# Optimization experiments

Hardware: AMD Instinct MI355X
Metric: run time of the kernel (lower is better)

## Reference

```python
import jax, jax.numpy as jnp
import numpy as np

EPS = 1e-6
H = 16  # num_heads

def _ln(x):
    mu = jnp.mean(x, axis=-1, keepdims=True)
    var = jnp.mean(jnp.square(x - mu), axis=-1, keepdims=True)
    return (x - mu) / jnp.sqrt(var + EPS)

def _mod(x, shift, scale):  # shift/scale: [B,D]
    return x * (1.0 + scale[:, None, :]) + shift[:, None, :]

def _heads(x, qkv_w, qkv_b):
    B, N, C = x.shape
    hd = C // H
    qkv = (x @ qkv_w + qkv_b).reshape(B, N, 3, H, hd).transpose(2, 0, 3, 1, 4)
    return qkv[0], qkv[1], qkv[2]  # each [B,H,N,hd]

def _attend(q, k, v):
    sc = (q.shape[-1]) ** -0.5
    a = jax.nn.softmax(jnp.einsum('bhnd,bhmd->bhnm', q, k) * sc, axis=-1)
    o = jnp.einsum('bhnm,bhmd->bhnd', a, v)
    B, h, N, hd = o.shape
    return o.transpose(0, 2, 1, 3).reshape(B, N, h * hd)

def _mha(x, qkv_w, qkv_b, proj_w, proj_b):
    q, k, v = _heads(x, qkv_w, qkv_b)
    return _attend(q, k, v) @ proj_w + proj_b

def setup_inputs() -> dict:
    key = jax.random.key(0)
    ks = jax.random.split(key, 16)
    B, T, D = 2, 2048, 1024
    Dh = 4 * D
    s = 0.02
    return {
        'x': jax.random.normal(ks[0], (B, T, D), jnp.float32),
        'c': jax.random.normal(ks[1], (B, 2, D), jnp.float32),
        'attn_qkv_w': jax.random.normal(ks[2], (D, 3 * D), jnp.float32) * s,
        'attn_qkv_b': jnp.zeros((3 * D,), jnp.float32),
        'attn_proj_w': jax.random.normal(ks[3], (D, D), jnp.float32) * s,
        'attn_proj_b': jnp.zeros((D,), jnp.float32),
        'crs_qkv_w': jax.random.normal(ks[4], (D, 3 * D), jnp.float32) * s,
        'crs_qkv_b': jnp.zeros((3 * D,), jnp.float32),
        'crs_proj_w': jax.random.normal(ks[5], (D, D), jnp.float32) * s,
        'crs_proj_b': jnp.zeros((D,), jnp.float32),
        'mlp_fc1_w': jax.random.normal(ks[6], (D, Dh), jnp.float32) * s,
        'mlp_fc1_b': jnp.zeros((Dh,), jnp.float32),
        'mlp_fc2_w': jax.random.normal(ks[7], (Dh, D), jnp.float32) * s,
        'mlp_fc2_b': jnp.zeros((D,), jnp.float32),
        'ada_w': jax.random.normal(ks[8], (D, 9 * D), jnp.float32) * s,
        'ada_b': jnp.zeros((9 * D,), jnp.float32),
    }

def reference(x, c, attn_qkv_w, attn_qkv_b, attn_proj_w, attn_proj_b,
              crs_qkv_w, crs_qkv_b, crs_proj_w, crs_proj_b,
              mlp_fc1_w, mlp_fc1_b, mlp_fc2_w, mlp_fc2_b, ada_w, ada_b):
    # adaLN-zero modulation: SiLU + Linear -> 9 chunks of [B,2,D]
    mod = jax.nn.silu(c) @ ada_w + ada_b
    (sh_msa, sc_msa, g_msa, sh_mca, sc_mca, g_mca,
     sh_mlp, sc_mlp, g_mlp) = jnp.split(mod, 9, axis=2)
    B, T, D = x.shape
    h = T // 2
    x0, x1 = x[:, :h], x[:, h:]
    # self-attention on each half with its own shift/scale/gate
    x0 = x0 + g_msa[:, 0][:, None, :] * _mha(_mod(_ln(x0), sh_msa[:, 0], sc_msa[:, 0]),
                                             attn_qkv_w, attn_qkv_b, attn_proj_w, attn_proj_b)
    x1 = x1 + g_msa[:, 1][:, None, :] * _mha(_mod(_ln(x1), sh_msa[:, 1], sc_msa[:, 1]),
                                             attn_qkv_w, attn_qkv_b, attn_proj_w, attn_proj_b)
    # two-way cross-attention
    xm = _mod(_ln(x0), sh_mca[:, 0], sc_mca[:, 0])
    ym = _mod(_ln(x1), sh_mca[:, 1], sc_mca[:, 1])
    qx, kx, vx = _heads(xm, crs_qkv_w, crs_qkv_b)
    qy, ky, vy = _heads(ym, crs_qkv_w, crs_qkv_b)
    ox = _attend(qx, ky, vy) @ crs_proj_w + crs_proj_b
    oy = _attend(qy, kx, vx) @ crs_proj_w + crs_proj_b
    x = x + jnp.concatenate((g_mca[:, 0][:, None, :] * ox,
                             g_mca[:, 1][:, None, :] * oy), axis=1)
    # gated MLP on each half
    def mlp(z):
        return jax.nn.gelu(z @ mlp_fc1_w + mlp_fc1_b, approximate=True) @ mlp_fc2_w + mlp_fc2_b
    m0 = mlp(_mod(_ln(x[:, :h]), sh_mlp[:, 0], sc_mlp[:, 0]))
    m1 = mlp(_mod(_ln(x[:, h:]), sh_mlp[:, 1], sc_mlp[:, 1]))
    x = x + jnp.concatenate((g_mlp[:, 0][:, None, :] * m0,
                             g_mlp[:, 1][:, None, :] * m1), axis=1)
    return x
```

## Files before the change

kernel.cpp:

```cpp
#include <hip/hip_runtime.h>
#include <hip/hip_bf16.h>

#define BB 2
#define TT 2048
#define DD 1024
#define NH 16
#define HALF 1024
#define DHID 4096
#define ND9 9216
#define ROWS (BB*TT)

using bf16 = __hip_bfloat16;
typedef short bf16x8 __attribute__((ext_vector_type(8)));
typedef float f32x4 __attribute__((ext_vector_type(4)));
typedef unsigned short u16;

__device__ __forceinline__ float b2f(bf16 v){ return __bfloat162float(v); }
__device__ __forceinline__ bf16 f2b(float v){ return __float2bfloat16(v); }
__device__ __forceinline__ float bits2f(u16 b){ return __uint_as_float(((unsigned)b) << 16); }
__device__ __forceinline__ u16 fb(float v){
    unsigned u = __float_as_uint(v);
    u += 0x7fffu + ((u >> 16) & 1u);
    return (u16)(u >> 16);
}
__device__ __forceinline__ void gl_lds16(const u16* g, u16* l) {
    __builtin_amdgcn_global_load_lds(
        (const __attribute__((address_space(1))) unsigned int*)g,
        (__attribute__((address_space(3))) unsigned int*)l, 16, 0, 0);
}

__global__ void ada_part(const float* __restrict__ c, const float* __restrict__ ada_w,
                         float* __restrict__ part) {
    __shared__ float sc_[4][64];
    int s = blockIdx.y;
    int k0 = s * 64;
    int n0 = blockIdx.x * 1024 + threadIdx.x * 4;
    {
        int r = threadIdx.x >> 6, k = threadIdx.x & 63;
        float v = c[r*DD + k0 + k];
        sc_[r][k] = v / (1.f + __expf(-v));
    }
    __syncthreads();
    float4 a0 = {0,0,0,0}, a1 = {0,0,0,0}, a2 = {0,0,0,0}, a3 = {0,0,0,0};
    for (int k = 0; k < 64; ++k) {
        float4 wv = *(const float4*)&ada_w[(size_t)(k0 + k)*ND9 + n0];
        float s0 = sc_[0][k], s1 = sc_[1][k], s2 = sc_[2][k], s3 = sc_[3][k];
        a0.x += s0*wv.x; a0.y += s0*wv.y; a0.z += s0*wv.z; a0.w += s0*wv.w;
        a1.x += s1*wv.x; a1.y += s1*wv.y; a1.z += s1*wv.z; a1.w += s1*wv.w;
        a2.x += s2*wv.x; a2.y += s2*wv.y; a2.z += s2*wv.z; a2.w += s2*wv.w;
        a3.x += s3*wv.x; a3.y += s3*wv.y; a3.z += s3*wv.z; a3.w += s3*wv.w;
    }
    *(float4*)&part[((size_t)(s*4 + 0))*ND9 + n0] = a0;
    *(float4*)&part[((size_t)(s*4 + 1))*ND9 + n0] = a1;
    *(float4*)&part[((size_t)(s*4 + 2))*ND9 + n0] = a2;
    *(float4*)&part[((size_t)(s*4 + 3))*ND9 + n0] = a3;
}

__global__ void ada_reduce(const float* __restrict__ part, const float* __restrict__ ada_b,
                           float* __restrict__ mod) {
    int g = blockIdx.x * 1024 + threadIdx.x * 4;
    int r = g / ND9, n = g - r*ND9;
    float4 acc = *(const float4*)&ada_b[n];
    #pragma unroll
    for (int s = 0; s < 16; ++s) {
        float4 p = *(const float4*)&part[((size_t)(s*4 + r))*ND9 + n];
        acc.x += p.x; acc.y += p.y; acc.z += p.z; acc.w += p.w;
    }
    *(float4*)&mod[(size_t)r*ND9 + n] = acc;
}

__global__ void cast_x4(const float* __restrict__ x, float* __restrict__ xc) {
    int i = (blockIdx.x * 256 + threadIdx.x) * 4;
    *(float4*)&xc[i] = *(const float4*)&x[i];
}

__global__ void resid_add(const float* __restrict__ src, const u16* __restrict__ gv,
                          float* __restrict__ dst) {
    int i = (blockIdx.x * 256 + threadIdx.x) * 4;
    float4 s = *(const float4*)&src[i];
    ushort4 g = *(const ushort4*)&gv[i];
    float4 o;
    o.x = s.x + bits2f(g.x); o.y = s.y + bits2f(g.y);
    o.z = s.z + bits2f(g.z); o.w = s.w + bits2f(g.w);
    *(float4*)&dst[i] = o;
}

__global__ void resid_ln(const float* __restrict__ src, const u16* __restrict__ gv,
                         const float* __restrict__ mod, int jshift, int jscale,
                         float* __restrict__ dstf, bf16* __restrict__ y) {
    int row = blockIdx.x;
    int b = row / TT, t = row % TT;
    int cz = (t >= HALF) ? 1 : 0;
    const float* mp = mod + (size_t)(b*2 + cz) * ND9;
    int tid = threadIdx.x;
    int d0 = tid * 4;
    float4 s = *(const float4*)&src[(size_t)row*DD + d0];
    float v[4] = {s.x, s.y, s.z, s.w};
    if (gv) {
        ushort4 g = *(const ushort4*)&gv[(size_t)row*DD + d0];
        v[0] += bits2f(g.x); v[1] += bits2f(g.y); v[2] += bits2f(g.z); v[3] += bits2f(g.w);
    }
    if (dstf) *(float4*)&dstf[(size_t)row*DD + d0] = (float4){v[0], v[1], v[2], v[3]};
    float sum = v[0]+v[1]+v[2]+v[3];
    float ssq = v[0]*v[0]+v[1]*v[1]+v[2]*v[2]+v[3]*v[3];
    __shared__ float red[256];
    red[tid] = sum; __syncthreads();
    for (int o = 128; o > 0; o >>= 1) { if (tid < o) red[tid] += red[tid+o]; __syncthreads(); }
    float mean = red[0] * (1.f/DD);
    __syncthreads();
    red[tid] = ssq; __syncthreads();
    for (int o = 128; o > 0; o >>= 1) { if (tid < o) red[tid] += red[tid+o]; __syncthreads(); }
    float var = red[0] * (1.f/DD) - mean*mean;
    float rstd = rsqrtf(var + 1e-6f);
    float4 sh = *(const float4*)&mp[jshift*DD + d0];
    float4 sc = *(const float4*)&mp[jscale*DD + d0];
    ushort4 o4;
    o4.x = fb((v[0]-mean)*rstd*(1.f+sc.x) + sh.x);
    o4.y = fb((v[1]-mean)*rstd*(1.f+sc.y) + sh.y);
    o4.z = fb((v[2]-mean)*rstd*(1.f+sc.z) + sh.z);
    o4.w = fb((v[3]-mean)*rstd*(1.f+sc.w) + sh.w);
    *(ushort4*)((u16*)y + (size_t)row*DD + d0) = o4;
}

__global__ void transpose_w(const float* __restrict__ W, u16* __restrict__ Wt, int K, int N) {
    __shared__ float T[32][33];
    int n0 = blockIdx.x * 32, k0 = blockIdx.y * 32;
    int lx = threadIdx.x & 31, ly = threadIdx.x >> 5;
    #pragma unroll
    for (int i = 0; i < 4; ++i)
        T[ly + i*8][lx] = W[(size_t)(k0 + ly + i*8)*N + n0 + lx];
    __syncthreads();
    #pragma unroll
    for (int i = 0; i < 4; ++i) {
        int n = ly + i*8;
        Wt[(size_t)(n0 + n)*K + k0 + lx] = fb(T[lx][n]);
    }
}

__global__ void vtrans(const u16* __restrict__ qkv, u16* __restrict__ vt) {
    __shared__ u16 T[64][72];
    int kt = blockIdx.x;
    int gh = blockIdx.y;
    int tid = threadIdx.x;
    int key = tid >> 2, c8 = (tid & 3) * 16;
    const u16* src = qkv + (size_t)((gh >> 4)*1024 + kt*64 + key)*3072 + 2048 + (gh & 15)*64 + c8;
    *(uint4*)&T[key][c8]     = *(const uint4*)src;
    *(uint4*)&T[key][c8 + 8] = *(const uint4*)(src + 8);
    __syncthreads();
    int d = tid >> 2, kc = (tid & 3) * 16;
    u16 tmp[16];
    #pragma unroll
    for (int i = 0; i < 16; ++i) tmp[i] = T[kc + i][d];
    u16* dst = vt + ((size_t)gh*64 + d)*1024 + kt*64 + kc;
    *(uint4*)&dst[0] = *(const uint4*)&tmp[0];
    *(uint4*)&dst[8] = *(const uint4*)&tmp[8];
}

__device__ __forceinline__ void epi_store(u16* out, int o_off, int N, int mm, int n, float v,
                                          const float* mod, int jg, int epi) {
    if (epi == 0) {
        out[(size_t)(mm - o_off)*N + n] = fb(v);
    } else if (epi == 1) {
        float z = 0.7978845608028654f*(v + 0.044715f*v*v*v);
        out[(size_t)(mm - o_off)*N + n] = fb(v / (1.f + __expf(-2.f*z)));
    } else {
        int brow = mm / TT, tt2 = mm % TT;
        int cz = (tt2 >= HALF) ? 1 : 0;
        const float* mp = mod + (size_t)(brow*2 + cz)*ND9 + (size_t)jg*DD;
        out[(size_t)(mm - o_off)*N + n] = fb(mp[n]*v);
    }
}

__global__ __launch_bounds__(256, 2) void gemm_mfma(
    const u16* __restrict__ A, const u16* __restrict__ Wt, const float* __restrict__ bias,
    u16* __restrict__ out, const float* __restrict__ mod, int jg,
    int m_base, int a_off, int o_off, int K, int N, int epi)
{
    __shared__ u16 As[128*64];
    __shared__ u16 Bs[128*64];
    int tid = threadIdx.x;
    int w = tid >> 6, lane = tid & 63;
    int quad = lane >> 4, l16 = lane & 15;
    int m0 = m_base + blockIdx.y * 128;
    int n0 = blockIdx.x * 128;
    int wr = (w & 1) * 64, wc = (w >> 1) * 64;

    f32x4 acc[4][4];
    #pragma unroll
    for (int i = 0; i < 4; ++i)
        #pragma unroll
        for (int j = 0; j < 4; ++j) acc[i][j] = (f32x4){0.f,0.f,0.f,0.f};

    const u16* Ag = A + (size_t)(m0 - a_off) * K;
    const u16* Bg = Wt + (size_t)n0 * K;
    int srow = lane >> 3;
    int scol = (((lane & 7) ^ ((lane >> 3) & 7))) * 8;
    int xsw = (l16 & 7);

    for (int k0 = 0; k0 < K; k0 += 64) {
        #pragma unroll
        for (int c = 0; c < 4; ++c) {
            int ch = w*4 + c;
            gl_lds16(Ag + (size_t)(ch*8 + srow)*K + k0 + scol, As + ch*512);
            gl_lds16(Bg + (size_t)(ch*8 + srow)*K + k0 + scol, Bs + ch*512);
        }
        __syncthreads();
        #pragma unroll
        for (int kk = 0; kk < 2; ++kk) {
            int pc = ((kk*4 + quad) ^ xsw) * 8;
            bf16x8 af[4], bfr[4];
            #pragma unroll
            for (int i = 0; i < 4; ++i) af[i] = *(const bf16x8*)&As[(wr + i*16 + l16)*64 + pc];
            #pragma unroll
            for (int j = 0; j < 4; ++j) bfr[j] = *(const bf16x8*)&Bs[(wc + j*16 + l16)*64 + pc];
            #pragma unroll
            for (int i = 0; i < 4; ++i)
                #pragma unroll
                for (int j = 0; j < 4; ++j)
                    acc[i][j] = __builtin_amdgcn_mfma_f32_16x16x32_bf16(af[i], bfr[j], acc[i][j], 0, 0, 0);
        }
        __syncthreads();
    }

    #pragma unroll
    for (int i = 0; i < 4; ++i)
        #pragma unroll
        for (int r = 0; r < 4; ++r) {
            int mm = m0 + wr + i*16 + quad*4 + r;
            #pragma unroll
            for (int j = 0; j < 4; ++j) {
                int n = n0 + wc + j*16 + l16;
                epi_store(out, o_off, N, mm, n, acc[i][j][r] + bias[n], mod, jg, epi);
            }
        }
}

__global__ __launch_bounds__(256, 2) void gemm64(
    const u16* __restrict__ A, const u16* __restrict__ Wt, const float* __restrict__ bias,
    u16* __restrict__ out, const float* __restrict__ mod, int jg,
    int m_base, int a_off, int o_off, int K, int N, int epi)
{
    __shared__ u16 As[64*64];
    __shared__ u16 Bs[128*64];
    int tid = threadIdx.x;
    int w = tid >> 6, lane = tid & 63;
    int quad = lane >> 4, l16 = lane & 15;
    int m0 = m_base + blockIdx.y * 64;
    int n0 = blockIdx.x * 128;

    f32x4 acc[4][2];
    #pragma unroll
    for (int i = 0; i < 4; ++i)
        #pragma unroll
        for (int j = 0; j < 2; ++j) acc[i][j] = (f32x4){0.f,0.f,0.f,0.f};

    const u16* Ag = A + (size_t)(m0 - a_off) * K;
    const u16* Bg = Wt + (size_t)n0 * K;
    int srow = lane >> 3;
    int scol = (((lane & 7) ^ ((lane >> 3) & 7))) * 8;
    int xsw = (l16 & 7);

    for (int k0 = 0; k0 < K; k0 += 64) {
        #pragma unroll
        for (int c = 0; c < 2; ++c) {
            int ch = w*2 + c;
            gl_lds16(Ag + (size_t)(ch*8 + srow)*K + k0 + scol, As + ch*512);
        }
        #pragma unroll
        for (int c = 0; c < 4; ++c) {
            int ch = w*4 + c;
            gl_lds16(Bg + (size_t)(ch*8 + srow)*K + k0 + scol, Bs + ch*512);
        }
        __syncthreads();
        #pragma unroll
        for (int kk = 0; kk < 2; ++kk) {
            int pc = ((kk*4 + quad) ^ xsw) * 8;
            bf16x8 af[4], bfr[2];
            #pragma unroll
            for (int i = 0; i < 4; ++i) af[i] = *(const bf16x8*)&As[(i*16 + l16)*64 + pc];
            #pragma unroll
            for (int j = 0; j < 2; ++j) bfr[j] = *(const bf16x8*)&Bs[(w*32 + j*16 + l16)*64 + pc];
            #pragma unroll
            for (int i = 0; i < 4; ++i)
                #pragma unroll
                for (int j = 0; j < 2; ++j)
                    acc[i][j] = __builtin_amdgcn_mfma_f32_16x16x32_bf16(af[i], bfr[j], acc[i][j], 0, 0, 0);
        }
        __syncthreads();
    }

    #pragma unroll
    for (int i = 0; i < 4; ++i)
        #pragma unroll
        for (int r = 0; r < 4; ++r) {
            int mm = m0 + i*16 + quad*4 + r;
            #pragma unroll
            for (int j = 0; j < 2; ++j) {
                int n = n0 + w*32 + j*16 + l16;
                epi_store(out, o_off, N, mm, n, acc[i][j][r] + bias[n], mod, jg, epi);
            }
        }
}

__global__ __launch_bounds__(256) void attn_mfma(const u16* __restrict__ qkv,
                                                 const u16* __restrict__ vt,
                                                 u16* __restrict__ attn_out, int kv_swap) {
    __shared__ u16 Ks[64][72];
    __shared__ u16 Vs[64][72];
    __shared__ u16 Ps[4][16][72];
    int qt = blockIdx.x, head = blockIdx.y, bh = blockIdx.z;
    int kvbh = kv_swap ? (bh ^ 1) : bh;
    int tid = threadIdx.x;
    int w = tid >> 6, lane = tid & 63;
    int quad = lane >> 4, l16 = lane & 15;
    int qrow0 = bh*1024 + qt*64 + w*16;

    const u16* qp = qkv + (size_t)(qrow0 + l16)*3072 + head*64;
    bf16x8 qa0 = *(const bf16x8*)(qp + quad*8);
    bf16x8 qa1 = *(const bf16x8*)(qp + 32 + quad*8);

    f32x4 oacc[4];
    #pragma unroll
    for (int i = 0; i < 4; ++i) oacc[i] = (f32x4){0.f,0.f,0.f,0.f};
    float mst[4], lst[4];
    #pragma unroll
    for (int r = 0; r < 4; ++r) { mst[r] = -3e38f; lst[r] = 0.f; }

    int skey = tid >> 2, sc8 = (tid & 3) * 16;
    const u16* kbase = qkv + (size_t)(kvbh*1024 + skey)*3072 + 1024 + head*64 + sc8;
    const u16* vbase = vt + ((size_t)(kvbh*16 + head)*64 + skey)*1024 + sc8;

    for (int kt = 0; kt < 16; ++kt) {
        __syncthreads();
        const u16* kp = kbase + (size_t)kt*64*3072;
        *(uint4*)&Ks[skey][sc8]     = *(const uint4*)kp;
        *(uint4*)&Ks[skey][sc8 + 8] = *(const uint4*)(kp + 8);
        const u16* vp = vbase + kt*64;
        *(uint4*)&Vs[skey][sc8]     = *(const uint4*)vp;
        *(uint4*)&Vs[skey][sc8 + 8] = *(const uint4*)(vp + 8);
        __syncthreads();

        f32x4 sacc[4];
        #pragma unroll
        for (int nt = 0; nt < 4; ++nt) sacc[nt] = (f32x4){0.f,0.f,0.f,0.f};
        #pragma unroll
        for (int nt = 0; nt < 4; ++nt) {
            bf16x8 kb0 = *(const bf16x8*)&Ks[nt*16 + l16][quad*8];
            bf16x8 kb1 = *(const bf16x8*)&Ks[nt*16 + l16][32 + quad*8];
            sacc[nt] = __builtin_amdgcn_mfma_f32_16x16x32_bf16(qa0, kb0, sacc[nt], 0, 0, 0);
            sacc[nt] = __builtin_amdgcn_mfma_f32_16x16x32_bf16(qa1, kb1, sacc[nt], 0, 0, 0);
        }
        #pragma unroll
        for (int r = 0; r < 4; ++r) {
            float sv0 = sacc[0][r]*0.125f, sv1 = sacc[1][r]*0.125f;
            float sv2 = sacc[2][r]*0.125f, sv3 = sacc[3][r]*0.125f;
            float mx = fmaxf(fmaxf(sv0, sv1), fmaxf(sv2, sv3));
            #pragma unroll
            for (int o = 1; o < 16; o <<= 1) mx = fmaxf(mx, __shfl_xor(mx, o));
            float mnew = fmaxf(mst[r], mx);
            float alpha = __expf(mst[r] - mnew);
            float p0 = __expf(sv0 - mnew), p1 = __expf(sv1 - mnew);
            float p2 = __expf(sv2 - mnew), p3 = __expf(sv3 - mnew);
            float ls = p0 + p1 + p2 + p3;
            #pragma unroll
            for (int o = 1; o < 16; o <<= 1) ls += __shfl_xor(ls, o);
            lst[r] = lst[r]*alpha + ls;
            mst[r] = mnew;
            #pragma unroll
            for (int dt = 0; dt < 4; ++dt) oacc[dt][r] *= alpha;
            int qr = quad*4 + r;
            Ps[w][qr][ 0 + l16] = fb(p0);
            Ps[w][qr][16 + l16] = fb(p1);
            Ps[w][qr][32 + l16] = fb(p2);
            Ps[w][qr][48 + l16] = fb(p3);
        }
        bf16x8 pa0 = *(const bf16x8*)&Ps[w][l16][quad*8];
        bf16x8 pa1 = *(const bf16x8*)&Ps[w][l16][32 + quad*8];
        #pragma unroll
        for (int dt = 0; dt < 4; ++dt) {
            bf16x8 vb0 = *(const bf16x8*)&Vs[dt*16 + l16][quad*8];
            bf16x8 vb1 = *(const bf16x8*)&Vs[dt*16 + l16][32 + quad*8];
            oacc[dt] = __builtin_amdgcn_mfma_f32_16x16x32_bf16(pa0, vb0, oacc[dt], 0, 0, 0);
            oacc[dt] = __builtin_amdgcn_mfma_f32_16x16x32_bf16(pa1, vb1, oacc[dt], 0, 0, 0);
        }
    }
    #pragma unroll
    for (int dt = 0; dt < 4; ++dt)
        #pragma unroll
        for (int r = 0; r < 4; ++r)
            attn_out[(size_t)(qrow0 + quad*4 + r)*DD + head*64 + dt*16 + l16] = fb(oacc[dt][r] / lst[r]);
}

extern "C" void kernel_launch(void* const* d_in, const int* in_sizes, int n_in,
                              void* d_out, int out_size, void* d_ws, size_t ws_size,
                              hipStream_t stream) {
    const float* x          = (const float*)d_in[0];
    const float* c          = (const float*)d_in[1];
    const float* attn_qkv_w = (const float*)d_in[2];
    const float* attn_qkv_b = (const float*)d_in[3];
    const float* attn_proj_w= (const float*)d_in[4];
    const float* attn_proj_b= (const float*)d_in[5];
    const float* crs_qkv_w  = (const float*)d_in[6];
    const float* crs_qkv_b  = (const float*)d_in[7];
    const float* crs_proj_w = (const float*)d_in[8];
    const float* crs_proj_b = (const float*)d_in[9];
    const float* fc1_w      = (const float*)d_in[10];
    const float* fc1_b      = (const float*)d_in[11];
    const float* fc2_w      = (const float*)d_in[12];
    const float* fc2_b      = (const float*)d_in[13];
    const float* ada_w      = (const float*)d_in[14];
    const float* ada_b      = (const float*)d_in[15];
    float* out = (float*)d_out;

    char* ws = (char*)d_ws;
    float* mod = (float*)ws;
    char* R1   = ws + (256u<<10);
    char* Yr   = R1 + (16u<<20);
    char* AOr  = Yr + (8u<<20);
    char* BIGr = AOr + (8u<<20);

    u16*   wt_a  = (u16*)R1;
    u16*   vt    = (u16*)(R1 + (8u<<20));
    bf16*  y     = (bf16*)Yr;
    u16*   wt_p  = (u16*)Yr;
    u16*   attn_o= (u16*)AOr;
    u16*   big   = (u16*)BIGr;
    u16*   gvB   = (u16*)BIGr;
    u16*   gvY   = (u16*)Yr;
    u16*   hstage= (u16*)AOr;
    u16*   fc1_t = (u16*)R1;
    u16*   fc2_t = (u16*)(R1 + (8u<<20));
    float* apart = (float*)BIGr;

    ada_part<<<dim3(9, 16), 256, 0, stream>>>(c, ada_w, apart);
    ada_reduce<<<36, 256, 0, stream>>>(apart, ada_b, mod);
    cast_x4<<<4096, 256, 0, stream>>>(x, out);

    transpose_w<<<dim3(3*DD/32, DD/32), 256, 0, stream>>>(attn_qkv_w, wt_a, DD, 3*DD);
    resid_ln<<<ROWS, 256, 0, stream>>>(out, nullptr, mod, 0, 1, nullptr, y);
    gemm_mfma<<<dim3(3*DD/128, ROWS/128), 256, 0, stream>>>((const u16*)y, wt_a, attn_qkv_b,
                                                            big, nullptr, 0, 0, 0, 0, DD, 3*DD, 0);
    vtrans<<<dim3(16, 64), 256, 0, stream>>>(big, vt);
    attn_mfma<<<dim3(16, NH, 4), 256, 0, stream>>>(big, vt, attn_o, 0);
    transpose_w<<<dim3(DD/32, DD/32), 256, 0, stream>>>(attn_proj_w, wt_p, DD, DD);
    gemm64<<<dim3(DD/128, ROWS/64), 256, 0, stream>>>(attn_o, wt_p, attn_proj_b,
                                                      gvB, mod, 2, 0, 0, 0, DD, DD, 3);
    resid_ln<<<ROWS, 256, 0, stream>>>(out, gvB, mod, 3, 4, nullptr, y);

    transpose_w<<<dim3(3*DD/32, DD/32), 256, 0, stream>>>(crs_qkv_w, wt_a, DD, 3*DD);
    gemm_mfma<<<dim3(3*DD/128, ROWS/128), 256, 0, stream>>>((const u16*)y, wt_a, crs_qkv_b,
                                                            big, nullptr, 0, 0, 0, 0, DD, 3*DD, 0);
    vtrans<<<dim3(16, 64), 256, 0, stream>>>(big, vt);
    attn_mfma<<<dim3(16, NH, 4), 256, 0, stream>>>(big, vt, attn_o, 1);
    transpose_w<<<dim3(DD/32, DD/32), 256, 0, stream>>>(crs_proj_w, wt_p, DD, DD);
    gemm64<<<dim3(DD/128, ROWS/64), 256, 0, stream>>>(attn_o, wt_p, crs_proj_b,
                                                      gvB, mod, 5, 0, 0, 0, DD, DD, 3);
    resid_ln<<<ROWS, 256, 0, stream>>>(out, gvB, mod, 6, 7, out, y);

    transpose_w<<<dim3(DHID/32, DD/32), 256, 0, stream>>>(fc1_w, fc1_t, DD, DHID);
    transpose_w<<<dim3(DD/32, DHID/32), 256, 0, stream>>>(fc2_w, fc2_t, DHID, DD);
    gemm_mfma<<<dim3(DHID/128, ROWS/128), 256, 0, stream>>>((const u16*)y, fc1_t, fc1_b,
                                                            hstage, nullptr, 0, 0, 0, 0, DD, DHID, 1);
    gemm64<<<dim3(DD/128, ROWS/64), 256, 0, stream>>>(hstage, fc2_t, fc2_b,
                                                      gvY, mod, 8, 0, 0, 0, DHID, DD, 3);
    resid_add<<<4096, 256, 0, stream>>>(out, gvY, out);
}
```

Measured before the change: 609.7 us.

## Prefetch K/V tiles into registers and transpose MFMA operands in attention

The attention kernel now loads the next K and V tiles from global memory into registers while the current tile is being computed, which hides global load latency behind the MFMA work. The QK^T and PV MFMAs swap operand order so that each lane holds a single query row. This turns the per-row softmax max and sum reductions from 4-step shuffles over 4 rows into 2-step shuffles over one row, and allows vectorised P and output stores. The grid axes of vtrans and attention are also reordered so that heads vary fastest, changing the order in which blocks touch memory. The cost is extra registers held live for the prefetched tiles.

```diff
diff --git a/kernel.cpp b/kernel.cpp
--- a/kernel.cpp
+++ b/kernel.cpp
@@ -139,8 +139,8 @@
 
 __global__ void vtrans(const u16* __restrict__ qkv, u16* __restrict__ vt) {
     __shared__ u16 T[64][72];
-    int kt = blockIdx.x;
-    int gh = blockIdx.y;
+    int kt = blockIdx.y;
+    int gh = blockIdx.x;
     int tid = threadIdx.x;
     int key = tid >> 2, c8 = (tid & 3) * 16;
     const u16* src = qkv + (size_t)((gh >> 4)*1024 + kt*64 + key)*3072 + 2048 + (gh & 15)*64 + c8;
@@ -308,7 +308,7 @@
     __shared__ u16 Ks[64][72];
     __shared__ u16 Vs[64][72];
     __shared__ u16 Ps[4][16][72];
-    int qt = blockIdx.x, head = blockIdx.y, bh = blockIdx.z;
+    int head = blockIdx.x, qt = blockIdx.y, bh = blockIdx.z;
     int kvbh = kv_swap ? (bh ^ 1) : bh;
     int tid = threadIdx.x;
     int w = tid >> 6, lane = tid & 63;
@@ -322,23 +322,32 @@
     f32x4 oacc[4];
     #pragma unroll
     for (int i = 0; i < 4; ++i) oacc[i] = (f32x4){0.f,0.f,0.f,0.f};
-    float mst[4], lst[4];
-    #pragma unroll
-    for (int r = 0; r < 4; ++r) { mst[r] = -3e38f; lst[r] = 0.f; }
+    float mst = -3e38f, lst = 0.f;
 
     int skey = tid >> 2, sc8 = (tid & 3) * 16;
     const u16* kbase = qkv + (size_t)(kvbh*1024 + skey)*3072 + 1024 + head*64 + sc8;
     const u16* vbase = vt + ((size_t)(kvbh*16 + head)*64 + skey)*1024 + sc8;
 
+    uint4 kr0 = *(const uint4*)kbase;
+    uint4 kr1 = *(const uint4*)(kbase + 8);
+    uint4 vr0 = *(const uint4*)vbase;
+    uint4 vr1 = *(const uint4*)(vbase + 8);
+
     for (int kt = 0; kt < 16; ++kt) {
         __syncthreads();
-        const u16* kp = kbase + (size_t)kt*64*3072;
-        *(uint4*)&Ks[skey][sc8]     = *(const uint4*)kp;
-        *(uint4*)&Ks[skey][sc8 + 8] = *(const uint4*)(kp + 8);
-        const u16* vp = vbase + kt*64;
-        *(uint4*)&Vs[skey][sc8]     = *(const uint4*)vp;
-        *(uint4*)&Vs[skey][sc8 + 8] = *(const uint4*)(vp + 8);
-        __syncthreads();
+        *(uint4*)&Ks[skey][sc8]     = kr0;
+        *(uint4*)&Ks[skey][sc8 + 8] = kr1;
+        *(uint4*)&Vs[skey][sc8]     = vr0;
+        *(uint4*)&Vs[skey][sc8 + 8] = vr1;
+        __syncthreads();
+        if (kt < 15) {
+            const u16* kp = kbase + (size_t)(kt + 1)*64*3072;
+            kr0 = *(const uint4*)kp;
+            kr1 = *(const uint4*)(kp + 8);
+            const u16* vp = vbase + (kt + 1)*64;
+            vr0 = *(const uint4*)vp;
+            vr1 = *(const uint4*)(vp + 8);
+        }
 
         f32x4 sacc[4];
         #pragma unroll
@@ -347,48 +356,57 @@
         for (int nt = 0; nt < 4; ++nt) {
             bf16x8 kb0 = *(const bf16x8*)&Ks[nt*16 + l16][quad*8];
             bf16x8 kb1 = *(const bf16x8*)&Ks[nt*16 + l16][32 + quad*8];
-            sacc[nt] = __builtin_amdgcn_mfma_f32_16x16x32_bf16(qa0, kb0, sacc[nt], 0, 0, 0);
-            sacc[nt] = __builtin_amdgcn_mfma_f32_16x16x32_bf16(qa1, kb1, sacc[nt], 0, 0, 0);
-        }
-        #pragma unroll
-        for (int r = 0; r < 4; ++r) {
-            float sv0 = sacc[0][r]*0.125f, sv1 = sacc[1][r]*0.125f;
-            float sv2 = sacc[2][r]*0.125f, sv3 = sacc[3][r]*0.125f;
-            float mx = fmaxf(fmaxf(sv0, sv1), fmaxf(sv2, sv3));
-            #pragma unroll
-            for (int o = 1; o < 16; o <<= 1) mx = fmaxf(mx, __shfl_xor(mx, o));
-            float mnew = fmaxf(mst[r], mx);
-            float alpha = __expf(mst[r] - mnew);
-            float p0 = __expf(sv0 - mnew), p1 = __expf(sv1 - mnew);
-            float p2 = __expf(sv2 - mnew), p3 = __expf(sv3 - mnew);
-            float ls = p0 + p1 + p2 + p3;
-            #pragma unroll
-            for (int o = 1; o < 16; o <<= 1) ls += __shfl_xor(ls, o);
-            lst[r] = lst[r]*alpha + ls;
-            mst[r] = mnew;
-            #pragma unroll
-            for (int dt = 0; dt < 4; ++dt) oacc[dt][r] *= alpha;
-            int qr = quad*4 + r;
-            Ps[w][qr][ 0 + l16] = fb(p0);
-            Ps[w][qr][16 + l16] = fb(p1);
-            Ps[w][qr][32 + l16] = fb(p2);
-            Ps[w][qr][48 + l16] = fb(p3);
-        }
+            sacc[nt] = __builtin_amdgcn_mfma_f32_16x16x32_bf16(kb0, qa0, sacc[nt], 0, 0, 0);
+            sacc[nt] = __builtin_amdgcn_mfma_f32_16x16x32_bf16(kb1, qa1, sacc[nt], 0, 0, 0);
+        }
+
+        float sv[4][4];
+        float tm = -3e38f;
+        #pragma unroll
+        for (int nt = 0; nt < 4; ++nt)
+            #pragma unroll
+            for (int r = 0; r < 4; ++r) {
+                sv[nt][r] = sacc[nt][r] * 0.125f;
+                tm = fmaxf(tm, sv[nt][r]);
+            }
+        tm = fmaxf(tm, __shfl_xor(tm, 16));
+        tm = fmaxf(tm, __shfl_xor(tm, 32));
+        float mnew = fmaxf(mst, tm);
+        float alpha = __expf(mst - mnew);
+        float ls = 0.f;
+        #pragma unroll
+        for (int nt = 0; nt < 4; ++nt) {
+            float p0 = __expf(sv[nt][0] - mnew), p1 = __expf(sv[nt][1] - mnew);
+            float p2 = __expf(sv[nt][2] - mnew), p3 = __expf(sv[nt][3] - mnew);
+            ls += (p0 + p1) + (p2 + p3);
+            ushort4 pk = {fb(p0), fb(p1), fb(p2), fb(p3)};
+            *(ushort4*)&Ps[w][l16][nt*16 + quad*4] = pk;
+        }
+        ls += __shfl_xor(ls, 16);
+        ls += __shfl_xor(ls, 32);
+        lst = lst*alpha + ls;
+        mst = mnew;
+        #pragma unroll
+        for (int dt = 0; dt < 4; ++dt)
+            #pragma unroll
+            for (int r = 0; r < 4; ++r) oacc[dt][r] *= alpha;
+
         bf16x8 pa0 = *(const bf16x8*)&Ps[w][l16][quad*8];
         bf16x8 pa1 = *(const bf16x8*)&Ps[w][l16][32 + quad*8];
         #pragma unroll
         for (int dt = 0; dt < 4; ++dt) {
             bf16x8 vb0 = *(const bf16x8*)&Vs[dt*16 + l16][quad*8];
             bf16x8 vb1 = *(const bf16x8*)&Vs[dt*16 + l16][32 + quad*8];
-            oacc[dt] = __builtin_amdgcn_mfma_f32_16x16x32_bf16(pa0, vb0, oacc[dt], 0, 0, 0);
-            oacc[dt] = __builtin_amdgcn_mfma_f32_16x16x32_bf16(pa1, vb1, oacc[dt], 0, 0, 0);
-        }
-    }
-    #pragma unroll
-    for (int dt = 0; dt < 4; ++dt)
-        #pragma unroll
-        for (int r = 0; r < 4; ++r)
-            attn_out[(size_t)(qrow0 + quad*4 + r)*DD + head*64 + dt*16 + l16] = fb(oacc[dt][r] / lst[r]);
+            oacc[dt] = __builtin_amdgcn_mfma_f32_16x16x32_bf16(vb0, pa0, oacc[dt], 0, 0, 0);
+            oacc[dt] = __builtin_amdgcn_mfma_f32_16x16x32_bf16(vb1, pa1, oacc[dt], 0, 0, 0);
+        }
+    }
+    float rl = 1.f / lst;
+    #pragma unroll
+    for (int dt = 0; dt < 4; ++dt) {
+        ushort4 o4 = {fb(oacc[dt][0]*rl), fb(oacc[dt][1]*rl), fb(oacc[dt][2]*rl), fb(oacc[dt][3]*rl)};
+        *(ushort4*)&attn_out[(size_t)(qrow0 + l16)*DD + head*64 + dt*16 + quad*4] = o4;
+    }
 }
 
 extern "C" void kernel_launch(void* const* d_in, const int* in_sizes, int n_in,
@@ -440,8 +458,8 @@
     resid_ln<<<ROWS, 256, 0, stream>>>(out, nullptr, mod, 0, 1, nullptr, y);
     gemm_mfma<<<dim3(3*DD/128, ROWS/128), 256, 0, stream>>>((const u16*)y, wt_a, attn_qkv_b,
                                                             big, nullptr, 0, 0, 0, 0, DD, 3*DD, 0);
-    vtrans<<<dim3(16, 64), 256, 0, stream>>>(big, vt);
-    attn_mfma<<<dim3(16, NH, 4), 256, 0, stream>>>(big, vt, attn_o, 0);
+    vtrans<<<dim3(64, 16), 256, 0, stream>>>(big, vt);
+    attn_mfma<<<dim3(NH, 16, 4), 256, 0, stream>>>(big, vt, attn_o, 0);
     transpose_w<<<dim3(DD/32, DD/32), 256, 0, stream>>>(attn_proj_w, wt_p, DD, DD);
     gemm64<<<dim3(DD/128, ROWS/64), 256, 0, stream>>>(attn_o, wt_p, attn_proj_b,
                                                       gvB, mod, 2, 0, 0, 0, DD, DD, 3);
@@ -450,8 +468,8 @@
     transpose_w<<<dim3(3*DD/32, DD/32), 256, 0, stream>>>(crs_qkv_w, wt_a, DD, 3*DD);
     gemm_mfma<<<dim3(3*DD/128, ROWS/128), 256, 0, stream>>>((const u16*)y, wt_a, crs_qkv_b,
                                                             big, nullptr, 0, 0, 0, 0, DD, 3*DD, 0);
-    vtrans<<<dim3(16, 64), 256, 0, stream>>>(big, vt);
-    attn_mfma<<<dim3(16, NH, 4), 256, 0, stream>>>(big, vt, attn_o, 1);
+    vtrans<<<dim3(64, 16), 256, 0, stream>>>(big, vt);
+    attn_mfma<<<dim3(NH, 16, 4), 256, 0, stream>>>(big, vt, attn_o, 1);
     transpose_w<<<dim3(DD/32, DD/32), 256, 0, stream>>>(crs_proj_w, wt_p, DD, DD);
     gemm64<<<dim3(DD/128, ROWS/64), 256, 0, stream>>>(attn_o, wt_p, crs_proj_b,
                                                       gvB, mod, 5, 0, 0, 0, DD, DD, 3);
```

Result: faster. 535.5 us (-12.2%).
